# Kernel tuning notes

Measured on AMD Instinct MI355X. Metric: run time of the kernel, lower is better.

The kernel has to match this reference:

```python
import jax, jax.numpy as jnp
import numpy as np

H = 4      # attention heads in HGTConv
DH = 32    # head dim
D = 128    # hidden size (rnn.hidden_size == hidden_size)
PAD = 0    # pad_idx


def setup_inputs() -> dict:
    key = jax.random.key(0)
    ks = jax.random.split(key, 16)
    Na = Np = 50000
    E = 800000
    V = 10000
    L = 8
    s = 0.05  # init scale keeps attention logits stable
    return {
        "tok_author": jax.random.randint(ks[0], (Na, L), 0, V),
        "tok_paper": jax.random.randint(ks[1], (Np, L), 0, V),
        "edge_ap": jax.random.randint(ks[2], (2, E), 0, Np),  # author -> paper
        "edge_pa": jax.random.randint(ks[3], (2, E), 0, Na),  # paper -> author
        "emb": jax.random.normal(ks[4], (V, D)) * s,
        "Wk": jax.random.normal(ks[5], (2, D, D)) * s,
        "Wq": jax.random.normal(ks[6], (2, D, D)) * s,
        "Wv": jax.random.normal(ks[7], (2, D, D)) * s,
        "Watt": jax.random.normal(ks[8], (2, H, DH, DH)) * s,
        "Wmsg": jax.random.normal(ks[9], (2, H, DH, DH)) * s,
        "mu": jnp.ones((2, H), jnp.float32),
        "Wout": jax.random.normal(ks[10], (2, D, D)) * s,
        "lin_w": jax.random.normal(ks[11], (D, D)) * s,
        "lin_b": jnp.zeros((D,), jnp.float32),
    }


def _st_encode(tok, emb):
    # STEncoder stand-in: embedding lookup, pad-masked mean pool, then relu_()
    e = emb[tok]                                   # [N, L, D]
    mask = (tok != PAD).astype(e.dtype)[..., None]  # [N, L, 1]
    pooled = (e * mask).sum(1) / jnp.maximum(mask.sum(1), 1.0)
    return jax.nn.relu(pooled)                     # [N, D]


def _segment_softmax(score, seg, n):
    m = jax.ops.segment_max(score, seg, num_segments=n)
    e = jnp.exp(score - m[seg])
    d = jax.ops.segment_sum(e, seg, num_segments=n)
    return e / (d[seg] + 1e-9)


def _proj(x, W):
    return (x @ W).reshape(x.shape[0], H, DH)


def _rel(k_src, v_src, q_dst, edges, Wa, Wm, mu_r, n_dst):
    # One HGT relation: per-edge key/message transform, segment-softmax attention,
    # scatter-add aggregation into destination nodes.
    src, dst = edges[0], edges[1]
    ke = jnp.einsum('ehd,hdf->ehf', k_src[src], Wa)           # [E, H, DH]
    score = (ke * q_dst[dst]).sum(-1) * mu_r / jnp.sqrt(jnp.float32(DH))  # [E, H]
    alpha = _segment_softmax(score, dst, n_dst)
    me = jnp.einsum('ehd,hdf->ehf', v_src[src], Wm)           # [E, H, DH]
    agg = jax.ops.segment_sum(alpha[..., None] * me, dst, num_segments=n_dst)
    return agg.reshape(n_dst, H * DH)


def reference(tok_author, tok_paper, edge_ap, edge_pa, emb, Wk, Wq, Wv,
              Watt, Wmsg, mu, Wout, lin_w, lin_b):
    # embed + relu per node type
    xa = _st_encode(tok_author, emb)   # [Na, D]
    xp = _st_encode(tok_paper, emb)    # [Np, D]
    Na = xa.shape[0]

    # per-node-type K/Q/V projections (type 0 = author, 1 = paper)
    ka, qa, va = _proj(xa, Wk[0]), _proj(xa, Wq[0]), _proj(xa, Wv[0])
    kp, qp, vp = _proj(xp, Wk[1]), _proj(xp, Wq[1]), _proj(xp, Wv[1])

    # only the 'author' node type feeds the output head, so we only need the
    # paper->author relation's aggregation (rel index 1)
    agg_a = _rel(kp, vp, qa, edge_pa, Watt[1], Wmsg[1], mu[1], Na)
    out_a = jax.nn.gelu(agg_a) @ Wout[0] + xa   # target-type linear + skip

    return out_a @ lin_w + lin_b
```

## Files before the change

kernel.cpp:

```cpp
#include <hip/hip_runtime.h>
#include <math.h>

#define L 8
#define FP8_SCALE 512.0f
#define FP8_INV   0.001953125f

typedef unsigned int  u32;
typedef unsigned short u16;
typedef __attribute__((ext_vector_type(8))) short bf16x8;
typedef __attribute__((ext_vector_type(4))) float f32x4;
typedef __attribute__((ext_vector_type(2))) float f32x2;

__device__ inline u16 f2bf(float x) {
    u32 u = __float_as_uint(x);
    return (u16)((u + 0x7fffu + ((u >> 16) & 1u)) >> 16);
}
__device__ inline float2 bf2f2(u32 v) {
    float2 r;
    r.x = __uint_as_float(v << 16);
    r.y = __uint_as_float(v & 0xffff0000u);
    return r;
}
__device__ inline float gelu_t(float x) {
    return 0.5f * x * (1.0f + tanhf(0.7978845608028654f *
           (x + 0.044715f * x * x * x)));
}

__device__ inline void zero_body(int bid, int tid, int* __restrict__ deg, int Na)
{
    int i = bid * 256 + tid;
    if (i < Na) deg[i] = 0;
}

__device__ inline void conv_emb_body(int bid, int tid,
    const float* __restrict__ emb, u32* __restrict__ emb_bf, int n2)
{
    int i = bid * 256 + tid;
    if (i >= n2) return;
    float2 e = *(const float2*)(emb + (size_t)i * 2);
    emb_bf[i] = ((u32)f2bf(e.y) << 16) | (u32)f2bf(e.x);
}

__device__ inline void hist_body8(int bid, int tid,
    const int* __restrict__ dstI, int* __restrict__ deg,
    int* __restrict__ rank, int E, int stride)
{
    int e0 = bid * 256 + tid;
    int d[8], r[8];
#pragma unroll
    for (int j = 0; j < 8; ++j) {
        int e = e0 + j * stride;
        d[j] = (e < E) ? dstI[e] : -1;
    }
#pragma unroll
    for (int j = 0; j < 8; ++j)
        r[j] = (d[j] >= 0) ? atomicAdd(&deg[d[j]], 1) : 0;
#pragma unroll
    for (int j = 0; j < 8; ++j) {
        int e = e0 + j * stride;
        if (d[j] >= 0) rank[e] = r[j];
    }
}

__device__ inline void fold_body(int bid, int tid,
    const float* __restrict__ Wk1, const float* __restrict__ Wq0,
    const float* __restrict__ Wv1, const float* __restrict__ Watt1,
    const float* __restrict__ Wmsg1, const float* __restrict__ Wout0,
    const float* __restrict__ lin_w,
    u16* __restrict__ wkaT, u16* __restrict__ wvmT,
    u16* __restrict__ wqT, u16* __restrict__ w1T, u16* __restrict__ lwT)
{
    int id = bid * 256 + tid;
    int which = id >> 14;
    int idx = id & 16383;
    int col = idx & 127;
    int k = idx >> 7;
    if (which == 0) {
        int h = col >> 5, f = col & 31;
        float s = 0.f;
        for (int d = 0; d < 32; ++d)
            s += Wk1[k * 128 + h * 32 + d] * Watt1[h * 1024 + d * 32 + f];
        wkaT[col * 128 + k] = f2bf(s);
    } else if (which == 1) {
        int h = col >> 5, f = col & 31;
        float s = 0.f;
        for (int d = 0; d < 32; ++d)
            s += Wv1[k * 128 + h * 32 + d] * Wmsg1[h * 1024 + d * 32 + f];
        wvmT[col * 128 + k] = f2bf(s);
    } else if (which == 2) {
        wqT[col * 128 + k] = f2bf(Wq0[k * 128 + col]);
    } else if (which == 3) {
        float s = 0.f;
        for (int d = 0; d < 128; ++d)
            s += Wout0[k * 128 + d] * lin_w[d * 128 + col];
        w1T[col * 128 + k] = f2bf(s);
    } else {
        lwT[col * 128 + k] = f2bf(lin_w[k * 128 + col]);
    }
}

__device__ inline void encode_body(int bid, int tid,
    const int* __restrict__ tok_a, const int* __restrict__ tok_p,
    const uint4* __restrict__ emb_bf4,
    uint4* __restrict__ xa4, uint4* __restrict__ xp4, int Na, int Ntot)
{
    int i = bid * 256 + tid;
    int n = i >> 4, q = i & 15;
    if (n >= Ntot) return;
    const int* tok = (n < Na) ? (tok_a + (size_t)n * L)
                              : (tok_p + (size_t)(n - Na) * L);
    int4 t0 = *(const int4*)tok;
    int4 t1 = *(const int4*)(tok + 4);
    int tt[8] = {t0.x, t0.y, t0.z, t0.w, t1.x, t1.y, t1.z, t1.w};
    float a[8] = {0.f, 0.f, 0.f, 0.f, 0.f, 0.f, 0.f, 0.f};
    int cnt = 0;
#pragma unroll
    for (int l = 0; l < L; ++l) {
        int t = tt[l];
        if (t != 0) {
            cnt++;
            uint4 e = emb_bf4[(size_t)t * 16 + q];
            float2 e0 = bf2f2(e.x), e1 = bf2f2(e.y);
            float2 e2 = bf2f2(e.z), e3 = bf2f2(e.w);
            a[0] += e0.x; a[1] += e0.y; a[2] += e1.x; a[3] += e1.y;
            a[4] += e2.x; a[5] += e2.y; a[6] += e3.x; a[7] += e3.y;
        }
    }
    float dn = 1.0f / fmaxf((float)cnt, 1.0f);
#pragma unroll
    for (int j = 0; j < 8; ++j) a[j] = fmaxf(a[j] * dn, 0.f);
    uint4 o;
    o.x = ((u32)f2bf(a[1]) << 16) | (u32)f2bf(a[0]);
    o.y = ((u32)f2bf(a[3]) << 16) | (u32)f2bf(a[2]);
    o.z = ((u32)f2bf(a[5]) << 16) | (u32)f2bf(a[4]);
    o.w = ((u32)f2bf(a[7]) << 16) | (u32)f2bf(a[6]);
    if (n < Na) xa4[(size_t)n * 16 + q] = o;
    else        xp4[(size_t)(n - Na) * 16 + q] = o;
}

__device__ inline void scatter_body8(int bid, int tid,
    const int* __restrict__ srcI, const int* __restrict__ dstI,
    const int* __restrict__ rank, const int* __restrict__ rowptr,
    int* __restrict__ csrc, int E, int stride)
{
    int e0 = bid * 256 + tid;
    int d[8], s[8], r[8];
#pragma unroll
    for (int j = 0; j < 8; ++j) {
        int e = e0 + j * stride;
        d[j] = (e < E) ? dstI[e] : -1;
        s[j] = (e < E) ? srcI[e] : 0;
        r[j] = (e < E) ? rank[e] : 0;
    }
    int base[8];
#pragma unroll
    for (int j = 0; j < 8; ++j)
        base[j] = (d[j] >= 0) ? rowptr[d[j]] : 0;
#pragma unroll
    for (int j = 0; j < 8; ++j)
        if (d[j] >= 0) csrc[base[j] + r[j]] = s[j];
}

__global__ __launch_bounds__(256) void k_zero_conv(
    int* deg, int Na, int Bzero,
    const float* emb, u32* emb_bf, int n2)
{
    int b = blockIdx.x, t = threadIdx.x;
    if (b < Bzero) zero_body(b, t, deg, Na);
    else           conv_emb_body(b - Bzero, t, emb, emb_bf, n2);
}

__global__ __launch_bounds__(256) void k_prep(
    const int* dstI, int* deg, int* rank, int E, int Bhist8, int stride,
    const float* Wk1, const float* Wq0, const float* Wv1,
    const float* Watt1, const float* Wmsg1, const float* Wout0,
    const float* lin_w, u16* wkaT, u16* wvmT, u16* wqT, u16* w1T, u16* lwT,
    int Bfold,
    const int* tok_a, const int* tok_p, const uint4* emb_bf4,
    uint4* xa4, uint4* xp4, int Na, int Ntot)
{
    int b = blockIdx.x, t = threadIdx.x;
    if (b < Bhist8)               hist_body8(b, t, dstI, deg, rank, E, stride);
    else if (b < Bhist8 + Bfold)  fold_body(b - Bhist8, t, Wk1, Wq0, Wv1,
                                      Watt1, Wmsg1, Wout0, lin_w,
                                      wkaT, wvmT, wqT, w1T, lwT);
    else encode_body(b - Bhist8 - Bfold, t, tok_a, tok_p, emb_bf4,
                     xa4, xp4, Na, Ntot);
}

__global__ __launch_bounds__(256) void k_scan(
    const int* __restrict__ deg, int* __restrict__ locpref,
    int* __restrict__ blocksum, int Na)
{
    __shared__ int lds[256];
    int tid = threadIdx.x;
    int base = blockIdx.x * 1024 + tid * 4;
    int4 v = {0, 0, 0, 0};
    if (base + 3 < Na) {
        v = *(const int4*)(deg + base);
    } else {
        if (base + 0 < Na) v.x = deg[base + 0];
        if (base + 1 < Na) v.y = deg[base + 1];
        if (base + 2 < Na) v.z = deg[base + 2];
        if (base + 3 < Na) v.w = deg[base + 3];
    }
    int tot = v.x + v.y + v.z + v.w;
    lds[tid] = tot;
    __syncthreads();
    for (int off = 1; off < 256; off <<= 1) {
        int u = (tid >= off) ? lds[tid - off] : 0;
        __syncthreads();
        lds[tid] += u;
        __syncthreads();
    }
    int excl = lds[tid] - tot;
    if (base < Na) {
        int4 o;
        o.x = excl;
        o.y = excl + v.x;
        o.z = o.y + v.y;
        o.w = o.z + v.z;
        if (base + 3 < Na) *(int4*)(locpref + base) = o;
        else {
            locpref[base] = o.x;
            if (base + 1 < Na) locpref[base + 1] = o.y;
            if (base + 2 < Na) locpref[base + 2] = o.z;
        }
    }
    if (tid == 255) blocksum[blockIdx.x] = lds[255];
}

__global__ __launch_bounds__(256) void k_final(
    const int* __restrict__ locpref, const int* __restrict__ blocksum,
    int* __restrict__ rowptr, int nb, int Na)
{
    __shared__ int lds[256];
    __shared__ int excl[256];
    int t = threadIdx.x;
    int s = (t < nb) ? blocksum[t] : 0;
    lds[t] = s;
    __syncthreads();
    for (int off = 1; off < 256; off <<= 1) {
        int u = (t >= off) ? lds[t - off] : 0;
        __syncthreads();
        lds[t] += u;
        __syncthreads();
    }
    excl[t] = lds[t] - s;
    __syncthreads();
    int i = blockIdx.x * 256 + t;
    if (i < Na)
        rowptr[i] = locpref[i] + excl[i >> 10];
    if (blockIdx.x == 0 && t == 0)
        rowptr[Na] = lds[nb - 1];
}

__global__ __launch_bounds__(256) void k_scat_proj(
    const int* srcI, const int* dstI, const int* rank, const int* rowptr,
    int* csrc, int E, int Bscat8, int stride,
    const u16* __restrict__ xa, const u16* __restrict__ xp,
    const u16* __restrict__ wqT, const u16* __restrict__ wkaT,
    const u16* __restrict__ wvmT,
    u16* __restrict__ qa, u32* __restrict__ km8, int Na, int Np, int gba,
    int Bproj)
{
    int b = blockIdx.x, t = threadIdx.x;
    if (b % 3 == 0) {
        int sb = b / 3;
        if (sb < Bscat8)
            scatter_body8(sb, t, srcI, dstI, rank, rowptr, csrc, E, stride);
        return;
    }
    int pb = (b / 3) * 2 + (b % 3 - 1);
    if (pb >= Bproj) return;

    int wave = t >> 6;
    int l = t & 63;
    int x = l & 15;
    int kb = (l >> 4) * 8;

    if (pb < gba) {
        int rbase = pb * 64 + wave * 16;
        int arow = rbase + x;
        if (arow >= Na) arow = Na - 1;
        bf16x8 af[4];
#pragma unroll
        for (int ks = 0; ks < 4; ++ks)
            af[ks] = *(const bf16x8*)(xa + (size_t)arow * 128 + ks * 32 + kb);
        f32x4 acc[8];
#pragma unroll
        for (int ct = 0; ct < 8; ++ct) acc[ct] = (f32x4){0.f, 0.f, 0.f, 0.f};
#pragma unroll
        for (int ks = 0; ks < 4; ++ks)
#pragma unroll
            for (int ct = 0; ct < 8; ++ct) {
                bf16x8 bf = *(const bf16x8*)(wqT + (size_t)(ct * 16 + x) * 128 + ks * 32 + kb);
                acc[ct] = __builtin_amdgcn_mfma_f32_16x16x32_bf16(af[ks], bf, acc[ct], 0, 0, 0);
            }
        int srow = rbase + ((l >> 4) << 2);
#pragma unroll
        for (int ct = 0; ct < 8; ++ct) {
            int col = ct * 16 + x;
#pragma unroll
            for (int r = 0; r < 4; ++r)
                if (srow + r < Na)
                    qa[(size_t)(srow + r) * 128 + col] = f2bf(acc[ct][r]);
        }
    } else {
        int b2 = pb - gba;
        int rbase = b2 * 64 + wave * 16;
        int arow = rbase + x;
        if (arow >= Np) arow = Np - 1;
        bf16x8 af[4];
#pragma unroll
        for (int ks = 0; ks < 4; ++ks)
            af[ks] = *(const bf16x8*)(xp + (size_t)arow * 128 + ks * 32 + kb);
        f32x4 kacc[8], macc[8];
#pragma unroll
        for (int ct = 0; ct < 8; ++ct) {
            kacc[ct] = (f32x4){0.f, 0.f, 0.f, 0.f};
            macc[ct] = (f32x4){0.f, 0.f, 0.f, 0.f};
        }
#pragma unroll
        for (int ks = 0; ks < 4; ++ks)
#pragma unroll
            for (int ct = 0; ct < 8; ++ct) {
                bf16x8 bk = *(const bf16x8*)(wkaT + (size_t)(ct * 16 + x) * 128 + ks * 32 + kb);
                kacc[ct] = __builtin_amdgcn_mfma_f32_16x16x32_bf16(af[ks], bk, kacc[ct], 0, 0, 0);
            }
#pragma unroll
        for (int ks = 0; ks < 4; ++ks)
#pragma unroll
            for (int ct = 0; ct < 8; ++ct) {
                bf16x8 bm = *(const bf16x8*)(wvmT + (size_t)(ct * 16 + x) * 128 + ks * 32 + kb);
                macc[ct] = __builtin_amdgcn_mfma_f32_16x16x32_bf16(af[ks], bm, macc[ct], 0, 0, 0);
            }
        int srow = rbase + ((l >> 4) << 2);
#pragma unroll
        for (int ct = 0; ct < 8; ++ct) {
#pragma unroll
            for (int r = 0; r < 4; ++r) {
                float k0 = kacc[ct][r] * FP8_SCALE;
                float k1 = __shfl_xor(k0, 1);
                float m0 = macc[ct][r] * FP8_SCALE;
                float m1 = __shfl_xor(m0, 1);
                if (!(x & 1) && (srow + r) < Np) {
                    int pk = __builtin_amdgcn_cvt_pk_fp8_f32(k0, k1, 0, false);
                    pk = __builtin_amdgcn_cvt_pk_fp8_f32(m0, m1, pk, true);
                    km8[(size_t)(srow + r) * 64 + ct * 8 + (x >> 1)] = (u32)pk;
                }
            }
        }
    }
}

__device__ inline void e_acc(u32 km, float2 qf, float muh,
                             float& dsum, float& a0, float& a1)
{
    f32x2 kf = __builtin_amdgcn_cvt_pk_f32_fp8(km, false);
    f32x2 mf = __builtin_amdgcn_cvt_pk_f32_fp8(km, true);
    float p = kf.x * qf.x + kf.y * qf.y;
    p += __shfl_xor(p, 1, 16);
    p += __shfl_xor(p, 2, 16);
    p += __shfl_xor(p, 4, 16);
    p += __shfl_xor(p, 8, 16);
    float ev = __expf(p * muh);
    dsum += ev; a0 += ev * mf.x; a1 += ev * mf.y;
}

__global__ __launch_bounds__(256) void csr_agg(
    const u32* __restrict__ km8, const u32* __restrict__ qap,
    const int* __restrict__ rowptr, const int* __restrict__ csrc,
    const float* __restrict__ mu1, u32* __restrict__ gagg, int Na)
{
    int dst = blockIdx.x * 4 + (threadIdx.x >> 6);
    if (dst >= Na) return;
    int lane = threadIdx.x & 63;
    int h = lane >> 4;
    float muh = mu1[h] * 0.17677669529663689f * FP8_INV;
    float2 qf = bf2f2(qap[(size_t)dst * 64 + lane]);

    float a0 = 0.f, a1 = 0.f, dsum = 0.f;
    int beg = rowptr[dst], end = rowptr[dst + 1];

    int i = beg;
    for (; i + 8 <= end; i += 8) {
        int s[8];
        u32 km[8];
#pragma unroll
        for (int j = 0; j < 8; ++j) s[j] = csrc[i + j];
#pragma unroll
        for (int j = 0; j < 8; ++j) km[j] = km8[(size_t)s[j] * 64 + lane];
#pragma unroll
        for (int j = 0; j < 8; ++j) e_acc(km[j], qf, muh, dsum, a0, a1);
    }
    for (; i + 4 <= end; i += 4) {
        int s0 = csrc[i], s1 = csrc[i + 1], s2 = csrc[i + 2], s3 = csrc[i + 3];
        u32 km0 = km8[(size_t)s0 * 64 + lane];
        u32 km1 = km8[(size_t)s1 * 64 + lane];
        u32 km2 = km8[(size_t)s2 * 64 + lane];
        u32 km3 = km8[(size_t)s3 * 64 + lane];
        e_acc(km0, qf, muh, dsum, a0, a1);
        e_acc(km1, qf, muh, dsum, a0, a1);
        e_acc(km2, qf, muh, dsum, a0, a1);
        e_acc(km3, qf, muh, dsum, a0, a1);
    }
    for (; i < end; ++i) {
        u32 km0 = km8[(size_t)csrc[i] * 64 + lane];
        e_acc(km0, qf, muh, dsum, a0, a1);
    }
    float dn = dsum + 1e-9f;
    a0 = gelu_t(a0 / dn * FP8_INV);
    a1 = gelu_t(a1 / dn * FP8_INV);
    gagg[(size_t)dst * 64 + lane] = ((u32)f2bf(a1) << 16) | (u32)f2bf(a0);
}

__global__ __launch_bounds__(256) void mfma_out(
    const u16* __restrict__ A0, const u16* __restrict__ WT0,
    const u16* __restrict__ A1, const u16* __restrict__ WT1,
    const float* __restrict__ bias, float* __restrict__ Y, int N)
{
    int wave = threadIdx.x >> 6;
    int l = threadIdx.x & 63;
    int rbase = blockIdx.x * 64 + wave * 16;
    int arow = rbase + (l & 15);
    if (arow >= N) arow = N - 1;
    int kb = (l >> 4) * 8;

    f32x4 acc[8];
#pragma unroll
    for (int ct = 0; ct < 8; ++ct) acc[ct] = (f32x4){0.f, 0.f, 0.f, 0.f};

    for (int w = 0; w < 2; ++w) {
        const u16* A  = w ? A1 : A0;
        const u16* WT = w ? WT1 : WT0;
        bf16x8 af[4];
#pragma unroll
        for (int ks = 0; ks < 4; ++ks)
            af[ks] = *(const bf16x8*)(A + (size_t)arow * 128 + ks * 32 + kb);
#pragma unroll
        for (int ks = 0; ks < 4; ++ks) {
#pragma unroll
            for (int ct = 0; ct < 8; ++ct) {
                bf16x8 bf = *(const bf16x8*)(WT + (size_t)(ct * 16 + (l & 15)) * 128 + ks * 32 + kb);
                acc[ct] = __builtin_amdgcn_mfma_f32_16x16x32_bf16(af[ks], bf, acc[ct], 0, 0, 0);
            }
        }
    }
    int srow = rbase + ((l >> 4) << 2);
#pragma unroll
    for (int ct = 0; ct < 8; ++ct) {
        int col = ct * 16 + (l & 15);
        float b = bias[col];
#pragma unroll
        for (int r = 0; r < 4; ++r) {
            if (srow + r < N)
                Y[(size_t)(srow + r) * 128 + col] = acc[ct][r] + b;
        }
    }
}

extern "C" void kernel_launch(void* const* d_in, const int* in_sizes, int n_in,
                              void* d_out, int out_size, void* d_ws, size_t ws_size,
                              hipStream_t stream)
{
    const int*   tok_a   = (const int*)d_in[0];
    const int*   tok_p   = (const int*)d_in[1];
    const int*   edge_pa = (const int*)d_in[3];
    const float* emb     = (const float*)d_in[4];
    const float* Wk      = (const float*)d_in[5];
    const float* Wq      = (const float*)d_in[6];
    const float* Wv      = (const float*)d_in[7];
    const float* Watt    = (const float*)d_in[8];
    const float* Wmsg    = (const float*)d_in[9];
    const float* mu      = (const float*)d_in[10];
    const float* Wout    = (const float*)d_in[11];
    const float* lin_w   = (const float*)d_in[12];
    const float* lin_b   = (const float*)d_in[13];

    int Na = in_sizes[0] / L;
    int Np = in_sizes[1] / L;
    int E  = in_sizes[3] / 2;
    int V  = in_sizes[4] / 128;
    float* out = (float*)d_out;

    u16* xa      = (u16*)d_ws;
    u16* qa      = xa + (size_t)Na * 128;
    u16* xp      = qa + (size_t)Na * 128;
    u16* gagg    = xp + (size_t)Np * 128;
    u16* emb_bf  = gagg + (size_t)Na * 128;
    u32* km8     = (u32*)(emb_bf + (size_t)V * 128);
    int* deg     = (int*)(km8 + (size_t)Np * 64);
    int* locpref = deg + Na;
    int* rowptr  = locpref + Na;
    int* csrc    = rowptr + Na + 2;
    int* blocksum= csrc + E;
    u16* wkaT    = (u16*)(blocksum + 256);
    u16* wvmT    = wkaT + 16384;
    u16* wqT     = wvmT + 16384;
    u16* w1T     = wqT + 16384;
    u16* lwT     = w1T + 16384;
    int* rank    = (int*)gagg;

    const int* e_src = edge_pa;
    const int* e_dst = edge_pa + E;

    int n2emb   = V * 64;
    int Bconv   = (n2emb + 255) / 256;
    int Bzero   = (Na + 255) / 256;
    int Bfold   = (5 * 16384) / 256;
    int Bhist8  = (E + 2047) / 2048;
    int hstride = Bhist8 * 256;
    int nb      = (Na + 1023) / 1024;
    int Ntot    = Na + Np;
    int Benc    = ((size_t)Ntot * 16 + 255) / 256;
    int BscanF  = (Na + 255) / 256;
    int gba     = (Na + 63) / 64;
    int gbp     = (Np + 63) / 64;
    int Bproj   = gba + gbp;
    int Bscat8  = (E + 2047) / 2048;
    int sstride = Bscat8 * 256;

    k_zero_conv<<<Bzero + Bconv, 256, 0, stream>>>(
        deg, Na, Bzero, emb, (u32*)emb_bf, n2emb);

    k_prep<<<Bhist8 + Bfold + Benc, 256, 0, stream>>>(
        e_dst, deg, rank, E, Bhist8, hstride,
        Wk + 16384, Wq, Wv + 16384, Watt + 4096, Wmsg + 4096, Wout, lin_w,
        wkaT, wvmT, wqT, w1T, lwT, Bfold,
        tok_a, tok_p, (const uint4*)emb_bf, (uint4*)xa, (uint4*)xp, Na, Ntot);

    k_scan<<<nb, 256, 0, stream>>>(deg, locpref, blocksum, Na);

    k_final<<<BscanF, 256, 0, stream>>>(locpref, blocksum, rowptr, nb, Na);

    int Gunit = (Bscat8 > (Bproj + 1) / 2) ? Bscat8 : (Bproj + 1) / 2;
    k_scat_proj<<<3 * Gunit, 256, 0, stream>>>(
        e_src, e_dst, rank, rowptr, csrc, E, Bscat8, sstride,
        xa, xp, wqT, wkaT, wvmT, qa, km8, Na, Np, gba, Bproj);

    csr_agg<<<(Na + 3) / 4, 256, 0, stream>>>(
        km8, (const u32*)qa, rowptr, csrc, mu + 4, (u32*)gagg, Na);

    mfma_out<<<gba, 256, 0, stream>>>(gagg, w1T, xa, lwT, lin_b, out, Na);
}
```

Before: 197.7 us.

## Fuse token encoding into projection kernel and stage output stores through LDS

Moves the embedding-lookup mean-pool encoder out of the prep kernel and into the projection blocks of the scatter/projection kernel. Each wave now encodes its own 16 rows into a shared-memory tile that feeds the MFMA A operand directly. The paper features xp are no longer written to or read back from global memory, and xa is still written because the output kernel needs it. The final output kernel also stages results in LDS so it can write coalesced float4 rows; this costs extra LDS space and can lower occupancy, and it makes the projection blocks heavier alongside the scatter blocks.

```diff
diff --git a/kernel.cpp b/kernel.cpp
--- a/kernel.cpp
+++ b/kernel.cpp
@@ -99,45 +99,6 @@
     }
 }
 
-__device__ inline void encode_body(int bid, int tid,
-    const int* __restrict__ tok_a, const int* __restrict__ tok_p,
-    const uint4* __restrict__ emb_bf4,
-    uint4* __restrict__ xa4, uint4* __restrict__ xp4, int Na, int Ntot)
-{
-    int i = bid * 256 + tid;
-    int n = i >> 4, q = i & 15;
-    if (n >= Ntot) return;
-    const int* tok = (n < Na) ? (tok_a + (size_t)n * L)
-                              : (tok_p + (size_t)(n - Na) * L);
-    int4 t0 = *(const int4*)tok;
-    int4 t1 = *(const int4*)(tok + 4);
-    int tt[8] = {t0.x, t0.y, t0.z, t0.w, t1.x, t1.y, t1.z, t1.w};
-    float a[8] = {0.f, 0.f, 0.f, 0.f, 0.f, 0.f, 0.f, 0.f};
-    int cnt = 0;
-#pragma unroll
-    for (int l = 0; l < L; ++l) {
-        int t = tt[l];
-        if (t != 0) {
-            cnt++;
-            uint4 e = emb_bf4[(size_t)t * 16 + q];
-            float2 e0 = bf2f2(e.x), e1 = bf2f2(e.y);
-            float2 e2 = bf2f2(e.z), e3 = bf2f2(e.w);
-            a[0] += e0.x; a[1] += e0.y; a[2] += e1.x; a[3] += e1.y;
-            a[4] += e2.x; a[5] += e2.y; a[6] += e3.x; a[7] += e3.y;
-        }
-    }
-    float dn = 1.0f / fmaxf((float)cnt, 1.0f);
-#pragma unroll
-    for (int j = 0; j < 8; ++j) a[j] = fmaxf(a[j] * dn, 0.f);
-    uint4 o;
-    o.x = ((u32)f2bf(a[1]) << 16) | (u32)f2bf(a[0]);
-    o.y = ((u32)f2bf(a[3]) << 16) | (u32)f2bf(a[2]);
-    o.z = ((u32)f2bf(a[5]) << 16) | (u32)f2bf(a[4]);
-    o.w = ((u32)f2bf(a[7]) << 16) | (u32)f2bf(a[6]);
-    if (n < Na) xa4[(size_t)n * 16 + q] = o;
-    else        xp4[(size_t)(n - Na) * 16 + q] = o;
-}
-
 __device__ inline void scatter_body8(int bid, int tid,
     const int* __restrict__ srcI, const int* __restrict__ dstI,
     const int* __restrict__ rank, const int* __restrict__ rowptr,
@@ -161,6 +122,49 @@
         if (d[j] >= 0) csrc[base[j] + r[j]] = s[j];
 }
 
+__device__ inline void enc_tile(
+    const int* __restrict__ tok, const uint4* __restrict__ emb_bf4,
+    u16 (* __restrict__ tile)[128], uint4* __restrict__ x4out,
+    int rbase, int N, int l)
+{
+    int g = l >> 4;
+    int q = l & 15;
+#pragma unroll
+    for (int p = 0; p < 4; ++p) {
+        int rl = p * 4 + g;
+        int row = rbase + rl;
+        int rc = (row < N) ? row : N - 1;
+        const int* tp = tok + (size_t)rc * L;
+        int4 t0 = *(const int4*)tp;
+        int4 t1 = *(const int4*)(tp + 4);
+        int tt[8] = {t0.x, t0.y, t0.z, t0.w, t1.x, t1.y, t1.z, t1.w};
+        float a[8] = {0.f, 0.f, 0.f, 0.f, 0.f, 0.f, 0.f, 0.f};
+        int cnt = 0;
+#pragma unroll
+        for (int j = 0; j < 8; ++j) {
+            int t = tt[j];
+            if (t != 0) {
+                cnt++;
+                uint4 e = emb_bf4[(size_t)t * 16 + q];
+                float2 e0 = bf2f2(e.x), e1 = bf2f2(e.y);
+                float2 e2 = bf2f2(e.z), e3 = bf2f2(e.w);
+                a[0] += e0.x; a[1] += e0.y; a[2] += e1.x; a[3] += e1.y;
+                a[4] += e2.x; a[5] += e2.y; a[6] += e3.x; a[7] += e3.y;
+            }
+        }
+        float dn = 1.0f / fmaxf((float)cnt, 1.0f);
+#pragma unroll
+        for (int j = 0; j < 8; ++j) a[j] = fmaxf(a[j] * dn, 0.f);
+        uint4 o;
+        o.x = ((u32)f2bf(a[1]) << 16) | (u32)f2bf(a[0]);
+        o.y = ((u32)f2bf(a[3]) << 16) | (u32)f2bf(a[2]);
+        o.z = ((u32)f2bf(a[5]) << 16) | (u32)f2bf(a[4]);
+        o.w = ((u32)f2bf(a[7]) << 16) | (u32)f2bf(a[6]);
+        *(uint4*)&tile[rl][q * 8] = o;
+        if (x4out && row < N) x4out[(size_t)row * 16 + q] = o;
+    }
+}
+
 __global__ __launch_bounds__(256) void k_zero_conv(
     int* deg, int Na, int Bzero,
     const float* emb, u32* emb_bf, int n2)
@@ -174,18 +178,12 @@
     const int* dstI, int* deg, int* rank, int E, int Bhist8, int stride,
     const float* Wk1, const float* Wq0, const float* Wv1,
     const float* Watt1, const float* Wmsg1, const float* Wout0,
-    const float* lin_w, u16* wkaT, u16* wvmT, u16* wqT, u16* w1T, u16* lwT,
-    int Bfold,
-    const int* tok_a, const int* tok_p, const uint4* emb_bf4,
-    uint4* xa4, uint4* xp4, int Na, int Ntot)
+    const float* lin_w, u16* wkaT, u16* wvmT, u16* wqT, u16* w1T, u16* lwT)
 {
     int b = blockIdx.x, t = threadIdx.x;
-    if (b < Bhist8)               hist_body8(b, t, dstI, deg, rank, E, stride);
-    else if (b < Bhist8 + Bfold)  fold_body(b - Bhist8, t, Wk1, Wq0, Wv1,
-                                      Watt1, Wmsg1, Wout0, lin_w,
-                                      wkaT, wvmT, wqT, w1T, lwT);
-    else encode_body(b - Bhist8 - Bfold, t, tok_a, tok_p, emb_bf4,
-                     xa4, xp4, Na, Ntot);
+    if (b < Bhist8) hist_body8(b, t, dstI, deg, rank, E, stride);
+    else fold_body(b - Bhist8, t, Wk1, Wq0, Wv1, Watt1, Wmsg1, Wout0,
+                   lin_w, wkaT, wvmT, wqT, w1T, lwT);
 }
 
 __global__ __launch_bounds__(256) void k_scan(
@@ -258,12 +256,14 @@
 __global__ __launch_bounds__(256) void k_scat_proj(
     const int* srcI, const int* dstI, const int* rank, const int* rowptr,
     int* csrc, int E, int Bscat8, int stride,
-    const u16* __restrict__ xa, const u16* __restrict__ xp,
+    const int* __restrict__ tok_a, const int* __restrict__ tok_p,
+    const uint4* __restrict__ emb_bf4, uint4* __restrict__ xa4,
     const u16* __restrict__ wqT, const u16* __restrict__ wkaT,
     const u16* __restrict__ wvmT,
     u16* __restrict__ qa, u32* __restrict__ km8, int Na, int Np, int gba,
     int Bproj)
 {
+    __shared__ u16 tile[4][16][128];
     int b = blockIdx.x, t = threadIdx.x;
     if (b % 3 == 0) {
         int sb = b / 3;
@@ -281,12 +281,11 @@
 
     if (pb < gba) {
         int rbase = pb * 64 + wave * 16;
-        int arow = rbase + x;
-        if (arow >= Na) arow = Na - 1;
+        enc_tile(tok_a, emb_bf4, tile[wave], xa4, rbase, Na, l);
         bf16x8 af[4];
 #pragma unroll
         for (int ks = 0; ks < 4; ++ks)
-            af[ks] = *(const bf16x8*)(xa + (size_t)arow * 128 + ks * 32 + kb);
+            af[ks] = *(const bf16x8*)&tile[wave][x][ks * 32 + kb];
         f32x4 acc[8];
 #pragma unroll
         for (int ct = 0; ct < 8; ++ct) acc[ct] = (f32x4){0.f, 0.f, 0.f, 0.f};
@@ -309,12 +308,11 @@
     } else {
         int b2 = pb - gba;
         int rbase = b2 * 64 + wave * 16;
-        int arow = rbase + x;
-        if (arow >= Np) arow = Np - 1;
+        enc_tile(tok_p, emb_bf4, tile[wave], nullptr, rbase, Np, l);
         bf16x8 af[4];
 #pragma unroll
         for (int ks = 0; ks < 4; ++ks)
-            af[ks] = *(const bf16x8*)(xp + (size_t)arow * 128 + ks * 32 + kb);
+            af[ks] = *(const bf16x8*)&tile[wave][x][ks * 32 + kb];
         f32x4 kacc[8], macc[8];
 #pragma unroll
         for (int ct = 0; ct < 8; ++ct) {
@@ -420,6 +418,7 @@
     const u16* __restrict__ A1, const u16* __restrict__ WT1,
     const float* __restrict__ bias, float* __restrict__ Y, int N)
 {
+    __shared__ float tile[4][16][128];
     int wave = threadIdx.x >> 6;
     int l = threadIdx.x & 63;
     int rbase = blockIdx.x * 64 + wave * 16;
@@ -447,15 +446,23 @@
             }
         }
     }
-    int srow = rbase + ((l >> 4) << 2);
 #pragma unroll
     for (int ct = 0; ct < 8; ++ct) {
         int col = ct * 16 + (l & 15);
         float b = bias[col];
 #pragma unroll
         for (int r = 0; r < 4; ++r) {
-            if (srow + r < N)
-                Y[(size_t)(srow + r) * 128 + col] = acc[ct][r] + b;
+            int rr = ((l >> 4) << 2) + r;
+            tile[wave][rr][col] = acc[ct][r] + b;
+        }
+    }
+#pragma unroll
+    for (int it = 0; it < 8; ++it) {
+        int rr = (l >> 5) + it * 2;
+        int row = rbase + rr;
+        if (row < N) {
+            float4 v = *(const float4*)&tile[wave][rr][(l & 31) * 4];
+            *(float4*)(Y + (size_t)row * 128 + (l & 31) * 4) = v;
         }
     }
 }
@@ -486,8 +493,7 @@
 
     u16* xa      = (u16*)d_ws;
     u16* qa      = xa + (size_t)Na * 128;
-    u16* xp      = qa + (size_t)Na * 128;
-    u16* gagg    = xp + (size_t)Np * 128;
+    u16* gagg    = qa + (size_t)Na * 128;
     u16* emb_bf  = gagg + (size_t)Na * 128;
     u32* km8     = (u32*)(emb_bf + (size_t)V * 128);
     int* deg     = (int*)(km8 + (size_t)Np * 64);
@@ -512,8 +518,6 @@
     int Bhist8  = (E + 2047) / 2048;
     int hstride = Bhist8 * 256;
     int nb      = (Na + 1023) / 1024;
-    int Ntot    = Na + Np;
-    int Benc    = ((size_t)Ntot * 16 + 255) / 256;
     int BscanF  = (Na + 255) / 256;
     int gba     = (Na + 63) / 64;
     int gbp     = (Np + 63) / 64;
@@ -524,11 +528,10 @@
     k_zero_conv<<<Bzero + Bconv, 256, 0, stream>>>(
         deg, Na, Bzero, emb, (u32*)emb_bf, n2emb);
 
-    k_prep<<<Bhist8 + Bfold + Benc, 256, 0, stream>>>(
+    k_prep<<<Bhist8 + Bfold, 256, 0, stream>>>(
         e_dst, deg, rank, E, Bhist8, hstride,
         Wk + 16384, Wq, Wv + 16384, Watt + 4096, Wmsg + 4096, Wout, lin_w,
-        wkaT, wvmT, wqT, w1T, lwT, Bfold,
-        tok_a, tok_p, (const uint4*)emb_bf, (uint4*)xa, (uint4*)xp, Na, Ntot);
+        wkaT, wvmT, wqT, w1T, lwT);
 
     k_scan<<<nb, 256, 0, stream>>>(deg, locpref, blocksum, Na);
 
@@ -537,7 +540,8 @@
     int Gunit = (Bscat8 > (Bproj + 1) / 2) ? Bscat8 : (Bproj + 1) / 2;
     k_scat_proj<<<3 * Gunit, 256, 0, stream>>>(
         e_src, e_dst, rank, rowptr, csrc, E, Bscat8, sstride,
-        xa, xp, wqT, wkaT, wvmT, qa, km8, Na, Np, gba, Bproj);
+        tok_a, tok_p, (const uint4*)emb_bf, (uint4*)xa,
+        wqT, wkaT, wvmT, qa, km8, Na, Np, gba, Bproj);
 
     csr_agg<<<(Na + 3) / 4, 256, 0, stream>>>(
         km8, (const u32*)qa, rowptr, csrc, mu + 4, (u32*)gagg, Na);
```

After: 205.8 us. 4.1% more time.
